# Kernel tuning notes

Hardware: AMD Instinct MI355X
Metric: run time of the kernel (lower is better)

The kernel has to match this reference:

```python
import jax, jax.numpy as jnp
import numpy as np

IN_DIM = 40
EMB = 20
HID = 20
T = 400000


def setup_inputs() -> dict:
    key = jax.random.key(0)
    ks = jax.random.split(key, 12)
    s_in = 1.0 / np.sqrt(IN_DIM)
    s_h = 1.0 / np.sqrt(HID)
    u = lambda k, shape, s: jax.random.uniform(k, shape, jnp.float32, -s, s)
    return {
        "in_states": jax.random.normal(ks[0], (T, IN_DIM), jnp.float32),
        "W_inp": u(ks[1], (EMB, IN_DIM), s_in),
        "b_inp": u(ks[2], (EMB,), s_in),
        "W_ih0": u(ks[3], (4 * HID, EMB), s_h),
        "W_hh0": u(ks[4], (4 * HID, HID), s_h),
        "b_ih0": u(ks[5], (4 * HID,), s_h),
        "b_hh0": u(ks[6], (4 * HID,), s_h),
        "W_ih1": u(ks[7], (4 * HID, HID), s_h),
        "W_hh1": u(ks[8], (4 * HID, HID), s_h),
        "b_ih1": u(ks[9], (4 * HID,), s_h),
        "b_hh1": u(ks[10], (4 * HID,), s_h),
        "W_out": u(ks[11], (1, HID), s_h),
        "b_out": jnp.zeros((1,), jnp.float32),
    }


def _lstm_cell(gates, h_prev, c_prev, W_hh):
    # PyTorch gate order: i, f, g, o
    g = gates + h_prev @ W_hh.T  # [4H]
    i = jax.nn.sigmoid(g[0 * HID:1 * HID])
    f = jax.nn.sigmoid(g[1 * HID:2 * HID])
    gg = jnp.tanh(g[2 * HID:3 * HID])
    o = jax.nn.sigmoid(g[3 * HID:4 * HID])
    c = f * c_prev + i * gg
    h = o * jnp.tanh(c)
    return h, c


def reference(in_states, W_inp, b_inp, W_ih0, W_hh0, b_ih0, b_hh0,
              W_ih1, W_hh1, b_ih1, b_hh1, W_out, b_out):
    # input projection for the whole sequence (big memory-bound GEMV batch)
    x = in_states @ W_inp.T + b_inp                       # [T, EMB]
    pre0 = x @ W_ih0.T + (b_ih0 + b_hh0)                  # [T, 4H]
    bias1 = b_ih1 + b_hh1

    def step(carry, pre0_t):
        h0, c0, h1, c1 = carry
        h0, c0 = _lstm_cell(pre0_t, h0, c0, W_hh0)
        gates1 = h0 @ W_ih1.T + bias1
        h1, c1 = _lstm_cell(gates1, h1, c1, W_hh1)
        return (h0, c0, h1, c1), h1

    z = jnp.zeros((HID,), in_states.dtype)
    (h0, c0, h1, c1), hs = jax.lax.scan(step, (z, z, z, z), pre0)
    outputs = (hs @ W_out.T + b_out).reshape(T, 1, 1)     # [T, 1, 1]
    h_n = jnp.stack([h0, h1])[:, None, :]                 # [2, 1, HID]
    c_n = jnp.stack([c0, c1])[:, None, :]
    return outputs, h_n, c_n
```

## Files before the change

kernel.cpp:

```cpp
#include <hip/hip_runtime.h>
#include <hip/hip_fp16.h>

#define T_LEN   400000
#define IN_DIM  40
#define EMB     20
#define HID     20
#define G4      80

#define CHUNK_L 64
#define NCHUNK  6250
#define NBLK    3125
#define WARM    48
#define WARMB   (WARM / 8)
#define NBATCH  ((CHUNK_L + WARM) / 8)

#define PRE0_TW 320
#define SD_STR  328
#define CBLK_H  (G4 * CHUNK_L)

#define PRE0_BYTE_OFF 32768

typedef _Float16 h2v __attribute__((ext_vector_type(2)));
typedef _Float16 h8v __attribute__((ext_vector_type(8)));
typedef float f32x4 __attribute__((ext_vector_type(4)));

#if __has_builtin(__builtin_amdgcn_fdot2)
#define FDOT2(a, b, c) __builtin_amdgcn_fdot2((a), (b), (c), false)
#else
#define FDOT2(a, b, c) ((float)(a)[0] * (float)(b)[0] + (float)(a)[1] * (float)(b)[1] + (c))
#endif

#if __has_builtin(__builtin_amdgcn_exp2f)
#define EXP2F(x) __builtin_amdgcn_exp2f(x)
#else
#define EXP2F(x) exp2f(x)
#endif
#if __has_builtin(__builtin_amdgcn_rcpf)
#define RCPF(x) __builtin_amdgcn_rcpf(x)
#else
#define RCPF(x) (1.0f / (x))
#endif

__device__ __forceinline__ float actg(float x, float c, float a, float b) {
  float e = EXP2F(c * x);
  float r = RCPF(1.f + e);
  return fmaf(a, r, b);
}
#define TANH_C (-2.885390082f)
#define SIGM_C (-1.442695041f)

#define WSYNC() do { __builtin_amdgcn_wave_barrier(); asm volatile("" ::: "memory"); } while (0)

__device__ __forceinline__ int orig_row(int r) { return (r & 3) * 20 + (r >> 2); }

__device__ __forceinline__ void loadrow_h(h2v* dst, const float* p) {
#pragma unroll
  for (int k = 0; k < 10; ++k) {
    h2v v; v[0] = (_Float16)p[2 * k]; v[1] = (_Float16)p[2 * k + 1];
    dst[k] = v;
  }
}

__device__ __forceinline__ void load10h(h2v* dst, const _Float16* base) {
  const uint4* p4 = (const uint4*)base;
  uint4 q0 = p4[0], q1 = p4[1];
  uint2 q2 = *(const uint2*)(base + 16);
  unsigned u[10] = {q0.x, q0.y, q0.z, q0.w, q1.x, q1.y, q1.z, q1.w, q2.x, q2.y};
#pragma unroll
  for (int k = 0; k < 10; ++k) dst[k] = __builtin_bit_cast(h2v, u[k]);
}

__device__ __forceinline__ h8v packh8(const float4& a, const float4& b) {
  __half2 p0 = __halves2half2(__float2half(a.x), __float2half(a.y));
  __half2 p1 = __halves2half2(__float2half(a.z), __float2half(a.w));
  __half2 p2 = __halves2half2(__float2half(b.x), __float2half(b.y));
  __half2 p3 = __halves2half2(__float2half(b.z), __float2half(b.w));
  uint4 u = make_uint4(*(unsigned*)&p0, *(unsigned*)&p1, *(unsigned*)&p2, *(unsigned*)&p3);
  return __builtin_bit_cast(h8v, u);
}

__global__ void prep_kernel(const float* __restrict__ W_inp, const float* __restrict__ b_inp,
                            const float* __restrict__ W_ih0, const float* __restrict__ b_ih0,
                            const float* __restrict__ b_hh0, const float* __restrict__ b_ih1,
                            const float* __restrict__ b_hh1, const float* __restrict__ W_out,
                            float* __restrict__ ws) {
  int tid = threadIdx.x;
  for (int idx = tid; idx < G4 * IN_DIM; idx += 256) {
    int r = idx / IN_DIM, j = idx % IN_DIM;
    int o = orig_row(r);
    float s = 0.f;
#pragma unroll
    for (int k = 0; k < EMB; ++k) s += W_ih0[o * EMB + k] * W_inp[k * IN_DIM + j];
    ws[idx] = s;
  }
  if (tid < G4) {
    int o = orig_row(tid);
    float s = b_ih0[o] + b_hh0[o];
#pragma unroll
    for (int k = 0; k < EMB; ++k) s += W_ih0[o * EMB + k] * b_inp[k];
    ws[3200 + tid] = s;
    ws[3280 + tid] = b_ih1[o] + b_hh1[o];
  }
  if (tid < 10) {
    __half2 p = __halves2half2(__float2half(W_out[2 * tid]), __float2half(W_out[2 * tid + 1]));
    ((unsigned*)ws)[3360 + tid] = *(unsigned*)&p;
  }
  __syncthreads();
  for (int i = tid; i < 2560; i += 256) {
    int r = i >> 5, kp = i & 31;
    unsigned v = 0;
    if (kp < 20) {
      __half2 p = __halves2half2(__float2half(ws[r * IN_DIM + 2 * kp]),
                                 __float2half(ws[r * IN_DIM + 2 * kp + 1]));
      v = *(unsigned*)&p;
    }
    ((unsigned*)ws)[5552 + i] = v;
  }
}

__global__ __launch_bounds__(256) void pre0_kernel(const float* __restrict__ in_states,
                                                   const float* __restrict__ ws,
                                                   __half* __restrict__ pre0c) {
  __shared__ __align__(16) _Float16 sD[80 * SD_STR];
  const int tid = threadIdx.x;
  const int l  = tid & 63;
  const int w  = tid >> 6;
  const int rb = l & 15;
  const int kg = l >> 4;
  const int t0 = blockIdx.x * PRE0_TW;
  const int tw = 80 * w;

  h8v afr[5][2];
  {
    const unsigned* wp = (const unsigned*)ws + 5552;
#pragma unroll
    for (int m = 0; m < 5; ++m)
#pragma unroll
      for (int ki = 0; ki < 2; ++ki) {
        uint4 q = *(const uint4*)&wp[(16 * m + rb) * 32 + 16 * ki + kg * 4];
        afr[m][ki] = __builtin_bit_cast(h8v, q);
      }
  }
  float4 bias4[5];
#pragma unroll
  for (int m = 0; m < 5; ++m) bias4[m] = *(const float4*)&ws[3200 + 16 * m + kg * 4];

#pragma unroll
  for (int n = 0; n < 5; ++n) {
    const int t = t0 + tw + 16 * n + rb;
    const float* xr = in_states + (size_t)t * IN_DIM;
    float4 x0 = *(const float4*)(xr + kg * 8);
    float4 x1 = *(const float4*)(xr + kg * 8 + 4);
    float4 y0 = make_float4(0.f, 0.f, 0.f, 0.f), y1 = y0;
    if (kg == 0) { y0 = *(const float4*)(xr + 32); y1 = *(const float4*)(xr + 36); }
    h8v b0 = packh8(x0, x1);
    h8v b1 = packh8(y0, y1);

    f32x4 acc[5];
#pragma unroll
    for (int m = 0; m < 5; ++m) {
      acc[m][0] = bias4[m].x; acc[m][1] = bias4[m].y;
      acc[m][2] = bias4[m].z; acc[m][3] = bias4[m].w;
    }
#pragma unroll
    for (int m = 0; m < 5; ++m) {
      acc[m] = __builtin_amdgcn_mfma_f32_16x16x32_f16(afr[m][0], b0, acc[m], 0, 0, 0);
      acc[m] = __builtin_amdgcn_mfma_f32_16x16x32_f16(afr[m][1], b1, acc[m], 0, 0, 0);
    }
#pragma unroll
    for (int m = 0; m < 5; ++m)
#pragma unroll
      for (int r = 0; r < 4; ++r)
        sD[(16 * m + kg * 4 + r) * SD_STR + tw + 16 * n + rb] = (_Float16)acc[m][r];
  }
  __syncthreads();

  for (int i = tid; i < 80 * (PRE0_TW / 8); i += 256) {
    int row = i / (PRE0_TW / 8);
    int q   = i % (PRE0_TW / 8);
    int j   = q >> 3;
    int o8  = q & 7;
    uint4 v = *(const uint4*)&sD[row * SD_STR + q * 8];
    *(uint4*)(pre0c + (size_t)(5 * blockIdx.x + j) * CBLK_H + row * CHUNK_L + o8 * 8) = v;
  }
}

__global__ __launch_bounds__(64, 2) void scan_kernel(
    const __half* __restrict__ pre0c, const float* __restrict__ ws,
    const float* __restrict__ W_hh0, const float* __restrict__ W_ih1,
    const float* __restrict__ W_hh1, const float* __restrict__ W_out,
    const float* __restrict__ b_out, float* __restrict__ out) {
  __shared__ __align__(16) float gp0s[2][96];
  __shared__ __align__(16) float r1ss[2][96];
  __shared__ __align__(16) float trashs[2][32];
  __shared__ __align__(16) _Float16 h0ss[2][32];
  __shared__ __align__(16) _Float16 h1ss[2][32];

  const int lane = threadIdx.x;
  const int l    = lane & 31;
  const int grp  = lane >> 5;
  const bool lo16 = (l < 16);

  const int chunk = blockIdx.x * 2 + grp;
  const int t0 = chunk * CHUNK_L - WARM;

  float* gp0 = gp0s[grp];
  float* r1s = r1ss[grp];
  _Float16* h0sg = h0ss[grp];
  _Float16* h1sg = h1ss[grp];

  h2v wG0a[10], wG0b[10], wR1a[10], wR1b[10], wS5[10], wI1a[10], wI1b[10], wS5c[10];
  loadrow_h(wG0a, W_hh0 + orig_row(l) * HID);
  loadrow_h(wG0b, W_hh0 + orig_row(l + 32) * HID);
  loadrow_h(wR1a, W_hh1 + orig_row(l) * HID);
  loadrow_h(wR1b, W_hh1 + orig_row(l + 32) * HID);
  loadrow_h(wS5, lo16 ? (W_hh0 + orig_row(64 + l) * HID)
                      : (W_hh1 + orig_row(64 + (l - 16)) * HID));
  loadrow_h(wI1a, W_ih1 + orig_row(l) * HID);
  loadrow_h(wI1b, W_ih1 + orig_row(l + 32) * HID);
  loadrow_h(wS5c, W_ih1 + orig_row(lo16 ? l : (64 + (l - 16))) * HID);
  h2v wouth[10];
  {
    const unsigned* woutp = (const unsigned*)ws + 3360;
#pragma unroll
    for (int k = 0; k < 10; ++k) wouth[k] = __builtin_bit_cast(h2v, woutp[k]);
  }
  const float b1a = ws[3280 + l];
  const float b1b = ws[3280 + l + 32];
  const float b1c = ws[3280 + 64 + (l & 15)];
  const float bout = b_out[0];

  const bool isT = ((l & 3) == 2);
  const float actC = isT ? TANH_C : SIGM_C;
  const float actA = isT ? 2.f : 1.f;
  const float actB = isT ? -1.f : 0.f;

  float* wr0 = &gp0[l];
  float* wr1 = &gp0[l + 32];
  float* wr4 = lo16 ? &gp0[64 + l] : &trashs[grp][l - 16];
  float* wc0 = &r1s[l];
  float* wc1 = &r1s[l + 32];
  float* wc4 = lo16 ? &trashs[grp][l] : &r1s[64 + (l - 16)];

  h2v hp0[10], hp1[10];
  {
    h2v z; z[0] = (_Float16)0.f; z[1] = (_Float16)0.f;
#pragma unroll
    for (int k = 0; k < 10; ++k) { hp0[k] = z; hp1[k] = z; }
  }
  float c0 = 0.f, c1 = 0.f, h0v = 0.f, h1v = 0.f;

  const int rowOffA = l * CHUNK_L;
  const int rowOffB = (l + 32) * CHUNK_L;
  const int rowOffC = (lo16 ? (64 + l) : (l + 32)) * CHUNK_L;
  const size_t blkC  = (size_t)chunk * CBLK_H;
  const size_t blkCm = (size_t)(chunk > 0 ? chunk - 1 : 0) * CBLK_H;
#define BBASE(b) (((b) < WARMB) ? (blkCm + 16 + 8 * (b)) : (blkC + 8 * ((b) - WARMB)))

  size_t base0 = BBASE(0);
  uint4 ua = *(const uint4*)(pre0c + base0 + rowOffA);
  uint4 ub = *(const uint4*)(pre0c + base0 + rowOffB);
  uint4 uc = *(const uint4*)(pre0c + base0 + rowOffC);

  for (int b = 0; b < NBATCH; ++b) {
    const int tb = t0 + 8 * b;
    const int bn = (b + 1 < NBATCH) ? b + 1 : b;
    const size_t nbase = BBASE(bn);
    uint4 na  = *(const uint4*)(pre0c + nbase + rowOffA);
    uint4 nb4 = *(const uint4*)(pre0c + nbase + rowOffB);
    uint4 nc4 = *(const uint4*)(pre0c + nbase + rowOffC);
    const bool upd = (tb >= 0);
    const bool live = (b >= WARMB);

#pragma unroll
    for (int s = 0; s < 8; ++s) {
      const float p_a = __half2float(((const __half*)&ua)[s]);
      const float p_b = __half2float(((const __half*)&ub)[s]);
      const float p_c = __half2float(((const __half*)&uc)[s]);

      float a0 = p_a, a1 = p_b;
      float r0 = b1a, r1v = b1b;
      float a4 = lo16 ? p_c : b1c;
#pragma unroll
      for (int k = 0; k < 10; ++k) {
        h2v hm = lo16 ? hp0[k] : hp1[k];
        a0  = FDOT2(wG0a[k], hp0[k], a0);
        a1  = FDOT2(wG0b[k], hp0[k], a1);
        r0  = FDOT2(wR1a[k], hp1[k], r0);
        r1v = FDOT2(wR1b[k], hp1[k], r1v);
        a4  = FDOT2(wS5[k],  hm, a4);
      }
      *wr0 = actg(a0, actC, actA, actB);
      *wr1 = actg(a1, actC, actA, actB);
      *wr4 = actg(a4, actC, actA, actB);
      WSYNC();

      if (l < 20) {
        float4 gv = ((const float4*)gp0)[l];
        float cn = fmaf(gv.y, c0, gv.x * gv.z);
        c0 = upd ? cn : c0;
        float tc = actg(c0, TANH_C, 2.f, -1.f);
        h0v = upd ? gv.w * tc : 0.f;
        h0sg[l] = (_Float16)h0v;
      }
      WSYNC();
      load10h(hp0, h0sg);

      float f0 = r0, f1 = r1v, f4 = a4;
#pragma unroll
      for (int k = 0; k < 10; ++k) {
        f0 = FDOT2(wI1a[k], hp0[k], f0);
        f1 = FDOT2(wI1b[k], hp0[k], f1);
        f4 = FDOT2(wS5c[k], hp0[k], f4);
      }
      *wc0 = actg(f0, actC, actA, actB);
      *wc1 = actg(f1, actC, actA, actB);
      *wc4 = actg(f4, actC, actA, actB);
      WSYNC();

      if (l < 20) {
        float4 gv = ((const float4*)r1s)[l];
        float cn = fmaf(gv.y, c1, gv.x * gv.z);
        c1 = upd ? cn : c1;
        float tc = actg(c1, TANH_C, 2.f, -1.f);
        h1v = upd ? gv.w * tc : 0.f;
        h1sg[l] = (_Float16)h1v;
      }
      WSYNC();
      load10h(hp1, h1sg);

      if (live) {
        float ov = bout;
#pragma unroll
        for (int k = 0; k < 10; ++k) ov = FDOT2(wouth[k], hp1[k], ov);
        if (l == 0) out[tb + s] = ov;
      }
    }
    ua = na; ub = nb4; uc = nc4;
  }

  if (blockIdx.x == NBLK - 1 && grp == 1 && l < 20) {
    out[T_LEN + l]      = h0v;
    out[T_LEN + 20 + l] = h1v;
    out[T_LEN + 40 + l] = c0;
    out[T_LEN + 60 + l] = c1;
  }
#undef BBASE
}

extern "C" void kernel_launch(void* const* d_in, const int* in_sizes, int n_in,
                              void* d_out, int out_size, void* d_ws, size_t ws_size,
                              hipStream_t stream) {
  const float* in_states = (const float*)d_in[0];
  const float* W_inp = (const float*)d_in[1];
  const float* b_inp = (const float*)d_in[2];
  const float* W_ih0 = (const float*)d_in[3];
  const float* W_hh0 = (const float*)d_in[4];
  const float* b_ih0 = (const float*)d_in[5];
  const float* b_hh0 = (const float*)d_in[6];
  const float* W_ih1 = (const float*)d_in[7];
  const float* W_hh1 = (const float*)d_in[8];
  const float* b_ih1 = (const float*)d_in[9];
  const float* b_hh1 = (const float*)d_in[10];
  const float* W_out = (const float*)d_in[11];
  const float* b_out = (const float*)d_in[12];

  float* ws = (float*)d_ws;
  __half* pre0c = (__half*)((char*)d_ws + PRE0_BYTE_OFF);
  float* outp = (float*)d_out;

  prep_kernel<<<1, 256, 0, stream>>>(W_inp, b_inp, W_ih0, b_ih0, b_hh0, b_ih1, b_hh1, W_out, ws);
  pre0_kernel<<<T_LEN / PRE0_TW, 256, 0, stream>>>(in_states, ws, pre0c);
  scan_kernel<<<NBLK, 64, 0, stream>>>(pre0c, ws, W_hh0, W_ih1, W_hh1, W_out, b_out, outp);
}
```

Baseline: 295.4 us.

## Store pre0 in 8-timestep slot layout and halve pre0 block size

Changes the intermediate pre0 buffer from per-chunk row-major blocks (80 rows x 64 timesteps) to contiguous 8-timestep slots (80 rows x 8), so each scan batch reads one compact 1280-byte slot instead of rows strided by 128 bytes. The pre0 kernel now uses 128-thread blocks covering 160 timesteps, which doubles the block count, and its write-out loop is reordered to emit slots contiguously. The aim is better coalescing and locality for the latency-bound scan loads and simpler warmup addressing. The risk is that per-warp tiling in pre0_kernel (tw = 80*w) must still fit the smaller block.

```diff
diff --git a/kernel.cpp b/kernel.cpp
--- a/kernel.cpp
+++ b/kernel.cpp
@@ -14,9 +14,9 @@
 #define WARMB   (WARM / 8)
 #define NBATCH  ((CHUNK_L + WARM) / 8)
 
-#define PRE0_TW 320
-#define SD_STR  328
-#define CBLK_H  (G4 * CHUNK_L)
+#define PRE0_TW 160
+#define SD_STR  168
+#define SLOT_H  (G4 * 8)
 
 #define PRE0_BYTE_OFF 32768
 
@@ -118,9 +118,9 @@
   }
 }
 
-__global__ __launch_bounds__(256) void pre0_kernel(const float* __restrict__ in_states,
+__global__ __launch_bounds__(128) void pre0_kernel(const float* __restrict__ in_states,
                                                    const float* __restrict__ ws,
-                                                   __half* __restrict__ pre0c) {
+                                                   __half* __restrict__ pre0b) {
   __shared__ __align__(16) _Float16 sD[80 * SD_STR];
   const int tid = threadIdx.x;
   const int l  = tid & 63;
@@ -175,18 +175,17 @@
   }
   __syncthreads();
 
-  for (int i = tid; i < 80 * (PRE0_TW / 8); i += 256) {
-    int row = i / (PRE0_TW / 8);
-    int q   = i % (PRE0_TW / 8);
-    int j   = q >> 3;
-    int o8  = q & 7;
+  for (int i = tid; i < (PRE0_TW / 8) * 80; i += 128) {
+    int q   = i / 80;
+    int row = i % 80;
+    size_t t8 = (size_t)blockIdx.x * (PRE0_TW / 8) + q;
     uint4 v = *(const uint4*)&sD[row * SD_STR + q * 8];
-    *(uint4*)(pre0c + (size_t)(5 * blockIdx.x + j) * CBLK_H + row * CHUNK_L + o8 * 8) = v;
+    *(uint4*)(pre0b + t8 * SLOT_H + row * 8) = v;
   }
 }
 
 __global__ __launch_bounds__(64, 2) void scan_kernel(
-    const __half* __restrict__ pre0c, const float* __restrict__ ws,
+    const __half* __restrict__ pre0b, const float* __restrict__ ws,
     const float* __restrict__ W_hh0, const float* __restrict__ W_ih1,
     const float* __restrict__ W_hh1, const float* __restrict__ W_out,
     const float* __restrict__ b_out, float* __restrict__ out) {
@@ -250,25 +249,23 @@
   }
   float c0 = 0.f, c1 = 0.f, h0v = 0.f, h1v = 0.f;
 
-  const int rowOffA = l * CHUNK_L;
-  const int rowOffB = (l + 32) * CHUNK_L;
-  const int rowOffC = (lo16 ? (64 + l) : (l + 32)) * CHUNK_L;
-  const size_t blkC  = (size_t)chunk * CBLK_H;
-  const size_t blkCm = (size_t)(chunk > 0 ? chunk - 1 : 0) * CBLK_H;
-#define BBASE(b) (((b) < WARMB) ? (blkCm + 16 + 8 * (b)) : (blkC + 8 * ((b) - WARMB)))
-
-  size_t base0 = BBASE(0);
-  uint4 ua = *(const uint4*)(pre0c + base0 + rowOffA);
-  uint4 ub = *(const uint4*)(pre0c + base0 + rowOffB);
-  uint4 uc = *(const uint4*)(pre0c + base0 + rowOffC);
+  const int rowOffA = l * 8;
+  const int rowOffB = (l + 32) * 8;
+  const int rowOffC = (lo16 ? (64 + l) : (l + 32)) * 8;
+#define SBASE(b) ((size_t)(((long)chunk * 8 - 6 + (b)) < 0 ? 0 : ((long)chunk * 8 - 6 + (b))) * SLOT_H)
+
+  size_t base0 = SBASE(0);
+  uint4 ua = *(const uint4*)(pre0b + base0 + rowOffA);
+  uint4 ub = *(const uint4*)(pre0b + base0 + rowOffB);
+  uint4 uc = *(const uint4*)(pre0b + base0 + rowOffC);
 
   for (int b = 0; b < NBATCH; ++b) {
     const int tb = t0 + 8 * b;
     const int bn = (b + 1 < NBATCH) ? b + 1 : b;
-    const size_t nbase = BBASE(bn);
-    uint4 na  = *(const uint4*)(pre0c + nbase + rowOffA);
-    uint4 nb4 = *(const uint4*)(pre0c + nbase + rowOffB);
-    uint4 nc4 = *(const uint4*)(pre0c + nbase + rowOffC);
+    const size_t nbase = SBASE(bn);
+    uint4 na  = *(const uint4*)(pre0b + nbase + rowOffA);
+    uint4 nb4 = *(const uint4*)(pre0b + nbase + rowOffB);
+    uint4 nc4 = *(const uint4*)(pre0b + nbase + rowOffC);
     const bool upd = (tb >= 0);
     const bool live = (b >= WARMB);
 
@@ -345,7 +342,7 @@
     out[T_LEN + 40 + l] = c0;
     out[T_LEN + 60 + l] = c1;
   }
-#undef BBASE
+#undef SBASE
 }
 
 extern "C" void kernel_launch(void* const* d_in, const int* in_sizes, int n_in,
@@ -366,10 +363,10 @@
   const float* b_out = (const float*)d_in[12];
 
   float* ws = (float*)d_ws;
-  __half* pre0c = (__half*)((char*)d_ws + PRE0_BYTE_OFF);
+  __half* pre0b = (__half*)((char*)d_ws + PRE0_BYTE_OFF);
   float* outp = (float*)d_out;
 
   prep_kernel<<<1, 256, 0, stream>>>(W_inp, b_inp, W_ih0, b_ih0, b_hh0, b_ih1, b_hh1, W_out, ws);
-  pre0_kernel<<<T_LEN / PRE0_TW, 256, 0, stream>>>(in_states, ws, pre0c);
-  scan_kernel<<<NBLK, 64, 0, stream>>>(pre0c, ws, W_hh0, W_ih1, W_hh1, W_out, b_out, outp);
-}
+  pre0_kernel<<<T_LEN / PRE0_TW, 128, 0, stream>>>(in_states, ws, pre0b);
+  scan_kernel<<<NBLK, 64, 0, stream>>>(pre0b, ws, W_hh0, W_ih1, W_hh1, W_out, b_out, outp);
+}
```

Measured after the change: 291.1 us. About the same (-1.4%).
